# Kernel tuning notes

Measured on AMD Instinct MI355X. Metric: run time of the kernel, lower is better.

The kernel has to match this reference:

```python
import math
import jax, jax.numpy as jnp
import numpy as np

EPS = 1e-6
N = 20000
KS = [256, 128, 64, 32]
DS = [1, 3, 5, 7]  # 2l+1 for l=0..3


def setup_inputs() -> dict:
    key = jax.random.key(0)
    ks = jax.random.split(key, 16)
    inp = {}
    for l, (d, k) in enumerate(zip(DS, KS)):
        inp[f"f{l}"] = jax.random.normal(ks[l], (N, d, d, k), dtype=jnp.float32)
        inp[f"wr{l}"] = jnp.ones((k,), dtype=jnp.float32)
        inp[f"wi{l}"] = jax.random.normal(ks[4 + l], (k, k), dtype=jnp.float32) / math.sqrt(k)
        inp[f"wo{l}"] = jax.random.normal(ks[8 + l], (k, k), dtype=jnp.float32) / math.sqrt(k)
    return inp


def _rmsnorm(x, w):
    # equivariant RMSNorm: RMS over uncoupled (i,j) dims and channels, per atom
    inv = jax.lax.rsqrt(jnp.mean(x * x, axis=(-3, -2, -1), keepdims=True) + EPS)
    return x * inv * w


def _linear(x, w):
    # channel mixing on last axis: [n,i,j,f] x [f,g] -> [n,i,j,g]
    return jnp.einsum('nijf,fg->nijg', x, w)


def _tp(u):
    # tensor product in uncoupled basis, per-channel matmul over (i,j)
    d = max(u.shape[-2], 1)
    return jnp.einsum('nijf,njkf->nikf', u, u) / math.sqrt(d)


def _cg_iter(f, wr, wi, wo):
    h = _linear(_rmsnorm(f, wr), wi)
    return f + _linear(_tp(h), wo)


def reference(f0, f1, f2, f3, wr0, wr1, wr2, wr3, wi0, wi1, wi2, wi3, wo0, wo1, wo2, wo3):
    feats = (f0, f1, f2, f3)
    wrs = (wr0, wr1, wr2, wr3)
    wis = (wi0, wi1, wi2, wi3)
    wos = (wo0, wo1, wo2, wo3)
    return tuple(_cg_iter(f, wr, wi, wo) for f, wr, wi, wo in zip(feats, wrs, wis, wos))
```

## Files before the change

kernel.cpp:

```cpp
#include <hip/hip_runtime.h>
#include <math.h>

#define BLOCK 256

typedef __attribute__((ext_vector_type(8))) short bf16x8;
typedef __attribute__((ext_vector_type(4))) float f32x4;
typedef __attribute__((ext_vector_type(16))) float f32x16;

static __device__ __forceinline__ unsigned short f2bf(float x) {
  unsigned u = __builtin_bit_cast(unsigned, x);
  u = (u + 0x7FFFu + ((u >> 16) & 1u)) >> 16;
  return (unsigned short)u;
}
static __device__ __forceinline__ float bf2f(unsigned short b) {
  return __builtin_bit_cast(float, (unsigned)b << 16);
}

typedef __attribute__((address_space(1))) unsigned int as1_t;
typedef __attribute__((address_space(3))) unsigned int as3_t;
static __device__ __forceinline__ void gl2lds16(const void* g, void* l) {
  __builtin_amdgcn_global_load_lds((const as1_t*)g, (as3_t*)l, 16, 0, 0);
}

__global__ __launch_bounds__(BLOCK) void prep_w(
    const float* __restrict__ w0, const float* __restrict__ w1,
    const float* __restrict__ w2, const float* __restrict__ w3,
    const float* __restrict__ w4, const float* __restrict__ w5,
    const float* __restrict__ w6, const float* __restrict__ w7,
    unsigned short* __restrict__ wsU)
{
  const int bpm[8]  = {64, 64, 16, 16, 4, 4, 1, 1};
  const int ks[8]   = {256, 256, 128, 128, 64, 64, 32, 32};
  const size_t doffE[8] = {0ull, 81920ull, 163840ull, 184320ull,
                           204800ull, 209920ull, 215040ull, 216576ull};
  const int cse[8] = {10240, 10240, 5120, 5120, 2560, 2560, 1536, 1536};
  const float* srcs[8] = {w0, w1, w2, w3, w4, w5, w6, w7};

  int m = 0, sub = blockIdx.x;
  while (m < 7 && sub >= bpm[m]) { sub -= bpm[m]; ++m; }
  const int K = ks[m];
  const int e = sub * 1024 + threadIdx.x * 4;
  const float4 v = *(const float4*)&srcs[m][e];
  const int k = e / K, c = e % K;
  const size_t d0 = doffE[m] + (size_t)(k >> 5) * cse[m] + (size_t)c * 40 + (k & 31);
  wsU[d0]       = f2bf(v.x);
  wsU[d0 + 40]  = f2bf(v.y);
  wsU[d0 + 80]  = f2bf(v.z);
  wsU[d0 + 120] = f2bf(v.w);
}

template<int K, int MP, int MR, int SX, int CG, int MODE, int CH, int PCH>
__device__ __forceinline__ void gemm_run(
    int tid, unsigned short* XB, const char* __restrict__ wsrc,
    const char* __restrict__ nextW, unsigned char* WT,
    const float* __restrict__ fres, float* __restrict__ outg, size_t obase)
{
  constexpr int RG = 4 / CG;
  constexpr int MT = MP / 32, NT = K / 32;
  constexpr int MTW = (MT + RG - 1) / RG, NTW = NT / CG;
  const int lane = tid & 63, wave = tid >> 6;
  const int wgn = wave % CG, wgm = wave / CG;
  const int rA = lane & 31, hA = lane >> 5;

  f32x16 acc[MTW][NTW] = {};

  for (int kc = 0; kc < CH; ++kc) {
    const unsigned short* W16 = (const unsigned short*)WT;
    bf16x8 bfr[NTW][2], afr[MTW][2];
#pragma unroll
    for (int ni = 0; ni < NTW; ++ni)
#pragma unroll
      for (int q = 0; q < 2; ++q)
        bfr[ni][q] = *(const bf16x8*)&W16[((wgn + ni * CG) * 32 + rA) * 40 + q * 16 + hA * 8];
#pragma unroll
    for (int mi = 0; mi < MTW; ++mi) {
      const int mt = wgm + mi * RG;
      if (mt < MT) {
#pragma unroll
        for (int q = 0; q < 2; ++q)
          afr[mi][q] = *(const bf16x8*)&XB[(mt * 32 + rA) * SX + kc * 32 + q * 16 + hA * 8];
      }
    }
    __syncthreads();

    if (kc + 1 < CH) {
      const char* sp = wsrc + (size_t)(kc + 1) * PCH;
      for (int o = wave * 1024; o < PCH; o += 4096)
        gl2lds16(sp + o + lane * 16, WT + o);
    } else if (nextW) {
      for (int o = wave * 1024; o < PCH; o += 4096)
        gl2lds16(nextW + o + lane * 16, WT + o);
    }

#pragma unroll
    for (int mi = 0; mi < MTW; ++mi) {
      const int mt = wgm + mi * RG;
      if (mt < MT) {
#pragma unroll
        for (int ni = 0; ni < NTW; ++ni)
#pragma unroll
          for (int q = 0; q < 2; ++q)
            acc[mi][ni] = __builtin_amdgcn_mfma_f32_32x32x16_bf16(
                afr[mi][q], bfr[ni][q], acc[mi][ni], 0, 0, 0);
      }
    }
    __syncthreads();
  }

#pragma unroll
  for (int mi = 0; mi < MTW; ++mi) {
    const int mt = wgm + mi * RG;
    if (mt >= MT) continue;
#pragma unroll
    for (int ni = 0; ni < NTW; ++ni) {
      const int col = (wgn + ni * CG) * 32 + rA;
#pragma unroll
      for (int r = 0; r < 16; ++r) {
        const int row = mt * 32 + (r & 3) + ((r >> 2) << 3) + (hA << 2);
        const float v = acc[mi][ni][r];
        if constexpr (MODE == 0) {
          if (row < MR) XB[row * SX + col] = f2bf(v);
        } else if constexpr (MODE == 2) {
          if (row < MR) XB[row * SX + col] = f2bf(v * v);
        } else {
          if (row < MR) {
            const size_t o = obase + (size_t)row * K + col;
            outg[o] = fres[o] + v;
          }
        }
      }
    }
  }
}

template<int K, int MP, int MR, int SX, int CG, int MODE, int CSE>
__device__ __forceinline__ void gemm_res(
    int tid, unsigned short* XB, const unsigned short* __restrict__ W16,
    const float* __restrict__ fres, float* __restrict__ outg, size_t obase)
{
  constexpr int RG = 4 / CG;
  constexpr int MT = MP / 32, NT = K / 32;
  constexpr int MTW = (MT + RG - 1) / RG, NTW = NT / CG;
  constexpr int CH = K / 32;
  const int lane = tid & 63, wave = tid >> 6;
  const int wgn = wave % CG, wgm = wave / CG;
  const int rA = lane & 31, hA = lane >> 5;

  f32x16 acc[MTW][NTW] = {};

#pragma unroll
  for (int kc = 0; kc < CH; ++kc) {
    const unsigned short* Wc = W16 + kc * CSE;
    bf16x8 bfr[NTW][2], afr[MTW][2];
#pragma unroll
    for (int ni = 0; ni < NTW; ++ni)
#pragma unroll
      for (int q = 0; q < 2; ++q)
        bfr[ni][q] = *(const bf16x8*)&Wc[((wgn + ni * CG) * 32 + rA) * 40 + q * 16 + hA * 8];
#pragma unroll
    for (int mi = 0; mi < MTW; ++mi) {
      const int mt = wgm + mi * RG;
      if (mt < MT) {
#pragma unroll
        for (int q = 0; q < 2; ++q)
          afr[mi][q] = *(const bf16x8*)&XB[(mt * 32 + rA) * SX + kc * 32 + q * 16 + hA * 8];
      }
    }
#pragma unroll
    for (int mi = 0; mi < MTW; ++mi) {
      const int mt = wgm + mi * RG;
      if (mt < MT) {
#pragma unroll
        for (int ni = 0; ni < NTW; ++ni)
#pragma unroll
          for (int q = 0; q < 2; ++q)
            acc[mi][ni] = __builtin_amdgcn_mfma_f32_32x32x16_bf16(
                afr[mi][q], bfr[ni][q], acc[mi][ni], 0, 0, 0);
      }
    }
  }

  if constexpr (MODE != 3) __syncthreads();

#pragma unroll
  for (int mi = 0; mi < MTW; ++mi) {
    const int mt = wgm + mi * RG;
    if (mt >= MT) continue;
#pragma unroll
    for (int ni = 0; ni < NTW; ++ni) {
      const int col = (wgn + ni * CG) * 32 + rA;
#pragma unroll
      for (int r = 0; r < 16; ++r) {
        const int row = mt * 32 + (r & 3) + ((r >> 2) << 3) + (hA << 2);
        const float v = acc[mi][ni][r];
        if constexpr (MODE == 0) {
          if (row < MR) XB[row * SX + col] = f2bf(v);
        } else if constexpr (MODE == 2) {
          if (row < MR) XB[row * SX + col] = f2bf(v * v);
        } else {
          if (row < MR) {
            const size_t o = obase + (size_t)row * K + col;
            outg[o] = fres[o] + v;
          }
        }
      }
    }
  }
}

template<int D, int K, int A, int MP, int CG, int CH, int PCH, int MODE1>
__device__ __forceinline__ void cg_body(
    int bid, const float* __restrict__ f, const float* __restrict__ wr,
    const char* __restrict__ wiw, const char* __restrict__ wow,
    float* __restrict__ out, unsigned char* SMEM)
{
  constexpr int DD  = D * D;
  constexpr int MR  = A * DD;
  constexpr int SX  = K + 8;
  constexpr int TPA = BLOCK / A;
  constexpr int NF4 = DD * K / 4;
  constexpr int CEIL = (NF4 + TPA - 1) / TPA;
  constexpr int XBB = MP * SX * 2;

  unsigned short* XB = (unsigned short*)SMEM;
  unsigned char*  WT = SMEM + XBB;

  const int tid = threadIdx.x, lane = tid & 63, wave = tid >> 6;
  const int nbase = bid * A;
  const size_t obase = (size_t)nbase * DD * K;

  for (int o = wave * 1024; o < PCH; o += 4096)
    gl2lds16(wiw + o + lane * 16, WT + o);

  const int a = tid / TPA, j = tid % TPA;
  const float* fa = f + (size_t)(nbase + a) * DD * K;
  float4 vreg[CEIL];
  float ss = 0.f;
#pragma unroll
  for (int it = 0; it < CEIL; ++it) {
    const int i = j + it * TPA;
    if (i < NF4) {
      vreg[it] = *(const float4*)&fa[i * 4];
      ss += vreg[it].x * vreg[it].x + vreg[it].y * vreg[it].y +
            vreg[it].z * vreg[it].z + vreg[it].w * vreg[it].w;
    }
  }
#pragma unroll
  for (int o = TPA >> 1; o >= 1; o >>= 1) ss += __shfl_xor(ss, o, 64);
  const float inv = rsqrtf(ss / (float)(DD * K) + 1e-6f);

#pragma unroll
  for (int it = 0; it < CEIL; ++it) {
    const int i = j + it * TPA;
    if (i < NF4) {
      const int e = i * 4, m = e / K, c = e % K;
      const float4 w4 = *(const float4*)&wr[c];
      const unsigned long long pk =
          (unsigned long long)f2bf(vreg[it].x * inv * w4.x) |
          ((unsigned long long)f2bf(vreg[it].y * inv * w4.y) << 16) |
          ((unsigned long long)f2bf(vreg[it].z * inv * w4.z) << 32) |
          ((unsigned long long)f2bf(vreg[it].w * inv * w4.w) << 48);
      *(unsigned long long*)&XB[(a * DD + m) * SX + c] = pk;
    }
  }
  __syncthreads();

  gemm_run<K, MP, MR, SX, CG, MODE1, CH, PCH>(
      tid, XB, wiw, wow, WT, nullptr, nullptr, 0);
  __syncthreads();

  if constexpr (D > 1) {
    const float rsD = rsqrtf((float)D);
    constexpr int PAIRS = A * K;
    if constexpr (PAIRS >= BLOCK) {
      static_assert(PAIRS % BLOCK == 0, "tp coverage");
#pragma unroll
      for (int it = 0; it < PAIRS / BLOCK; ++it) {
        const int p = tid + it * BLOCK;
        const int aa = p / K, c = p % K;
        float hv[DD];
#pragma unroll
        for (int r = 0; r < DD; ++r) hv[r] = bf2f(XB[(aa * DD + r) * SX + c]);
#pragma unroll
        for (int i2 = 0; i2 < D; ++i2)
#pragma unroll
          for (int k2 = 0; k2 < D; ++k2) {
            float s = 0.f;
#pragma unroll
            for (int jj = 0; jj < D; ++jj) s += hv[i2 * D + jj] * hv[jj * D + k2];
            XB[(aa * DD + i2 * D + k2) * SX + c] = f2bf(s * rsD);
          }
      }
    } else {
      static_assert(PAIRS * 2 == BLOCK, "tp two-lane coverage");
      const int p = tid >> 1, half = tid & 1;
      const int aa = p / K, c = p % K;
      float hv[DD];
#pragma unroll
      for (int r = 0; r < DD; ++r) hv[r] = bf2f(XB[(aa * DD + r) * SX + c]);
      const int i0 = half ? (D / 2 + 1) : 0;
      const int i1 = half ? D : (D / 2 + 1);
      for (int i2 = i0; i2 < i1; ++i2)
#pragma unroll
        for (int k2 = 0; k2 < D; ++k2) {
          float s = 0.f;
#pragma unroll
          for (int jj = 0; jj < D; ++jj) s += hv[i2 * D + jj] * hv[jj * D + k2];
          XB[(aa * DD + i2 * D + k2) * SX + c] = f2bf(s * rsD);
        }
    }
    __syncthreads();
  }

  gemm_run<K, MP, MR, SX, CG, 3, CH, PCH>(
      tid, XB, wow, nullptr, WT, f, out, obase);
}

template<int D, int K, int A, int MP, int CG, int CSE, int WIB, int WOB>
__device__ __forceinline__ void cg_body_res(
    int bid, const float* __restrict__ f, const float* __restrict__ wr,
    const char* __restrict__ wiw, const char* __restrict__ wow,
    float* __restrict__ out, unsigned char* SMEM)
{
  constexpr int DD  = D * D;
  constexpr int MR  = A * DD;
  constexpr int SX  = K + 8;
  constexpr int TPA = BLOCK / A;
  constexpr int NF4 = DD * K / 4;
  constexpr int CEIL = (NF4 + TPA - 1) / TPA;
  constexpr int XBB = MP * SX * 2;

  unsigned short* XB = (unsigned short*)SMEM;
  unsigned char*  W  = SMEM + XBB;

  const int tid = threadIdx.x, lane = tid & 63, wave = tid >> 6;
  const int nbase = bid * A;
  const size_t obase = (size_t)nbase * DD * K;

  for (int o = wave * 1024; o < WIB; o += 4096)
    gl2lds16(wiw + o + lane * 16, W + o);
  for (int o = wave * 1024; o < WOB; o += 4096)
    gl2lds16(wow + o + lane * 16, W + WIB + o);

  const int a = tid / TPA, j = tid % TPA;
  const float* fa = f + (size_t)(nbase + a) * DD * K;
  float4 vreg[CEIL];
  float ss = 0.f;
#pragma unroll
  for (int it = 0; it < CEIL; ++it) {
    const int i = j + it * TPA;
    if (i < NF4) {
      vreg[it] = *(const float4*)&fa[i * 4];
      ss += vreg[it].x * vreg[it].x + vreg[it].y * vreg[it].y +
            vreg[it].z * vreg[it].z + vreg[it].w * vreg[it].w;
    }
  }
#pragma unroll
  for (int o = TPA >> 1; o >= 1; o >>= 1) ss += __shfl_xor(ss, o, 64);
  const float inv = rsqrtf(ss / (float)(DD * K) + 1e-6f);

#pragma unroll
  for (int it = 0; it < CEIL; ++it) {
    const int i = j + it * TPA;
    if (i < NF4) {
      const int e = i * 4, m = e / K, c = e % K;
      const float4 w4 = *(const float4*)&wr[c];
      const unsigned long long pk =
          (unsigned long long)f2bf(vreg[it].x * inv * w4.x) |
          ((unsigned long long)f2bf(vreg[it].y * inv * w4.y) << 16) |
          ((unsigned long long)f2bf(vreg[it].z * inv * w4.z) << 32) |
          ((unsigned long long)f2bf(vreg[it].w * inv * w4.w) << 48);
      *(unsigned long long*)&XB[(a * DD + m) * SX + c] = pk;
    }
  }
  __syncthreads();

  gemm_res<K, MP, MR, SX, CG, 0, CSE>(
      tid, XB, (const unsigned short*)W, nullptr, nullptr, 0);
  __syncthreads();

  {
    const float rsD = rsqrtf((float)D);
    constexpr int PAIRS = A * K;
    if constexpr (PAIRS >= BLOCK) {
      static_assert(PAIRS % BLOCK == 0, "tp coverage");
#pragma unroll
      for (int it = 0; it < PAIRS / BLOCK; ++it) {
        const int p = tid + it * BLOCK;
        const int aa = p / K, c = p % K;
        float hv[DD];
#pragma unroll
        for (int r = 0; r < DD; ++r) hv[r] = bf2f(XB[(aa * DD + r) * SX + c]);
#pragma unroll
        for (int i2 = 0; i2 < D; ++i2)
#pragma unroll
          for (int k2 = 0; k2 < D; ++k2) {
            float s = 0.f;
#pragma unroll
            for (int jj = 0; jj < D; ++jj) s += hv[i2 * D + jj] * hv[jj * D + k2];
            XB[(aa * DD + i2 * D + k2) * SX + c] = f2bf(s * rsD);
          }
      }
    } else {
      static_assert(PAIRS * 2 == BLOCK, "tp two-lane coverage");
      const int p = tid >> 1, half = tid & 1;
      const int aa = p / K, c = p % K;
      float hv[DD];
#pragma unroll
      for (int r = 0; r < DD; ++r) hv[r] = bf2f(XB[(aa * DD + r) * SX + c]);
      const int i0 = half ? (D / 2 + 1) : 0;
      const int i1 = half ? D : (D / 2 + 1);
      for (int i2 = i0; i2 < i1; ++i2)
#pragma unroll
        for (int k2 = 0; k2 < D; ++k2) {
          float s = 0.f;
#pragma unroll
          for (int jj = 0; jj < D; ++jj) s += hv[i2 * D + jj] * hv[jj * D + k2];
          XB[(aa * DD + i2 * D + k2) * SX + c] = f2bf(s * rsD);
        }
    }
  }
  __syncthreads();

  gemm_res<K, MP, MR, SX, CG, 3, CSE>(
      tid, XB, (const unsigned short*)(W + WIB), f, out, obase);
}

__global__ __launch_bounds__(BLOCK, 3) void cg_mega(
    const float* __restrict__ f0, const float* __restrict__ wr0,
    const float* __restrict__ f1, const float* __restrict__ wr1,
    const float* __restrict__ f2, const float* __restrict__ wr2,
    const float* __restrict__ f3, const float* __restrict__ wr3,
    const char* __restrict__ wsB,
    float* __restrict__ out0, float* __restrict__ out1,
    float* __restrict__ out2, float* __restrict__ out3)
{
  __shared__ __align__(16) unsigned char SMEM[53760];
  const int b = blockIdx.x;
  if (b < 625) {
    cg_body<1, 256, 32,  32, 4, 8, 20480, 2>(
        b, f0, wr0, wsB + 0, wsB + 163840, out0, SMEM);
  } else if (b < 1875) {
    cg_body<3, 128, 16, 160, 4, 4, 10240, 0>(
        b - 625, f1, wr1, wsB + 327680, wsB + 368640, out1, SMEM);
  } else if (b < 4375) {
    cg_body_res<5,  64, 8, 224, 2, 2560, 10240, 10240>(
        b - 1875, f2, wr2, wsB + 409600, wsB + 419840, out2, SMEM);
  } else {
    cg_body_res<7,  32, 8, 416, 1, 1536,  3072,  3072>(
        b - 4375, f3, wr3, wsB + 430080, wsB + 433152, out3, SMEM);
  }
}

template<int K, int MP, int MR, int SX, int SH, int WGM, int WGN, int MTW, int NTW, bool FINAL>
__device__ __forceinline__ void fb_gemm(
    int tid, const unsigned short* __restrict__ XB, float* __restrict__ Hs,
    unsigned short* __restrict__ WTl, const float* __restrict__ Wg,
    const float* __restrict__ fres, float* __restrict__ out, size_t obase)
{
  constexpr int TM = MP / 16;
  constexpr int WSTR = 40;
  const int lane = tid & 63;
  const int wave = tid >> 6;
  const int wgn = wave % WGN;
  const int wgm = wave / WGN;
  const int rl = lane & 15;
  const int kl = (lane >> 4) * 8;
  const int rit = (lane >> 4) * 4;
  const int cit = lane & 15;

  f32x4 acc[MTW][NTW];
#pragma unroll
  for (int mi = 0; mi < MTW; ++mi)
#pragma unroll
    for (int ni = 0; ni < NTW; ++ni) acc[mi][ni] = f32x4{0.f, 0.f, 0.f, 0.f};

  for (int kc = 0; kc < K / 32; ++kc) {
    __syncthreads();
    for (int i = tid; i < 32 * K; i += BLOCK) {
      const int kk = i / K, c = i % K;
      WTl[c * WSTR + kk] = f2bf(Wg[(size_t)(kc * 32 + kk) * K + c]);
    }
    __syncthreads();
    bf16x8 bfr[NTW], afr[MTW];
#pragma unroll
    for (int ni = 0; ni < NTW; ++ni) {
      const int col = (wgn + ni * WGN) * 16 + rl;
      bfr[ni] = *(const bf16x8*)&WTl[col * WSTR + kl];
    }
#pragma unroll
    for (int mi = 0; mi < MTW; ++mi) {
      const int mt = wgm + mi * WGM;
      if (mt < TM) afr[mi] = *(const bf16x8*)&XB[(mt * 16 + rl) * SX + kc * 32 + kl];
    }
#pragma unroll
    for (int mi = 0; mi < MTW; ++mi) {
      const int mt = wgm + mi * WGM;
      if (mt < TM) {
#pragma unroll
        for (int ni = 0; ni < NTW; ++ni)
          acc[mi][ni] = __builtin_amdgcn_mfma_f32_16x16x32_bf16(afr[mi], bfr[ni], acc[mi][ni], 0, 0, 0);
      }
    }
  }
#pragma unroll
  for (int mi = 0; mi < MTW; ++mi) {
    const int mt = wgm + mi * WGM;
    if (mt >= TM) continue;
#pragma unroll
    for (int ni = 0; ni < NTW; ++ni) {
      const int col = (wgn + ni * WGN) * 16 + cit;
#pragma unroll
      for (int r = 0; r < 4; ++r) {
        const int row = mt * 16 + rit + r;
        if constexpr (!FINAL) {
          Hs[row * SH + col] = acc[mi][ni][r];
        } else {
          if (row < MR) {
            const size_t o = obase + (size_t)row * K + col;
            out[o] = fres[o] + acc[mi][ni][r];
          }
        }
      }
    }
  }
}

template<int D, int K, int A, int MP, int WGM, int WGN, int MTW, int NTW>
__global__ __launch_bounds__(BLOCK) void cg_mfma_fb(
    const float* __restrict__ f, const float* __restrict__ wr,
    const float* __restrict__ wi, const float* __restrict__ wo,
    float* __restrict__ out)
{
  constexpr int DD = D * D;
  constexpr int MR = A * DD;
  constexpr int SX = K + 8;
  constexpr int SH = K + 4;
  constexpr int TPA = BLOCK / A;
  constexpr int WSTR = 40;

  __shared__ __align__(16) unsigned short XB[MP * SX];
  __shared__ __align__(16) float H[MP * SH];
  __shared__ __align__(16) unsigned short WTl[K * WSTR];
  __shared__ float s_inv[A];

  const int tid = threadIdx.x;
  const int nbase = blockIdx.x * A;
  const size_t obase = (size_t)nbase * DD * K;

  if constexpr (MP > MR) {
    for (int i = tid; i < (MP - MR) * K; i += BLOCK)
      XB[(MR + i / K) * SX + (i % K)] = 0;
  }
  {
    const int a = tid / TPA, j = tid % TPA;
    const float4* fap = (const float4*)(f + (size_t)(nbase + a) * DD * K);
    constexpr int NF4 = DD * K / 4;
    float ss = 0.f;
    for (int i = j; i < NF4; i += TPA) {
      const float4 v = fap[i];
      const int e = i * 4, m = e / K, c = e % K;
      *(float4*)&H[(a * DD + m) * SH + c] = v;
      ss += v.x * v.x + v.y * v.y + v.z * v.z + v.w * v.w;
    }
#pragma unroll
    for (int o = TPA >> 1; o >= 1; o >>= 1) ss += __shfl_xor(ss, o, 64);
    if (j == 0) s_inv[a] = rsqrtf(ss / (float)(DD * K) + 1e-6f);
  }
  __syncthreads();
  for (int i2 = tid; i2 < MR * K / 2; i2 += BLOCK) {
    const int e = i2 * 2, m = e / K, c = e % K;
    const float2 v = *(const float2*)&H[m * SH + c];
    const float2 wv = *(const float2*)&wr[c];
    const float s = s_inv[m / DD];
    const unsigned lo = f2bf(v.x * s * wv.x);
    const unsigned hi = f2bf(v.y * s * wv.y);
    *(unsigned*)&XB[m * SX + c] = lo | (hi << 16);
  }
  fb_gemm<K, MP, MR, SX, SH, WGM, WGN, MTW, NTW, false>(
      tid, XB, H, WTl, wi, nullptr, nullptr, 0);
  __syncthreads();
  {
    const float rsD = rsqrtf((float)D);
    for (int base = 0; base < A * K; base += BLOCK) {
      const int t2 = base + tid;
      if (t2 < A * K) {
        const int aa = t2 / K, c = t2 % K;
        float hv[DD];
#pragma unroll
        for (int r = 0; r < DD; ++r) hv[r] = H[(aa * DD + r) * SH + c];
#pragma unroll
        for (int i = 0; i < D; ++i)
#pragma unroll
          for (int k2 = 0; k2 < D; ++k2) {
            float s = 0.f;
#pragma unroll
            for (int jj = 0; jj < D; ++jj) s += hv[i * D + jj] * hv[jj * D + k2];
            XB[(aa * DD + i * D + k2) * SX + c] = f2bf(s * rsD);
          }
      }
    }
  }
  fb_gemm<K, MP, MR, SX, SH, WGM, WGN, MTW, NTW, true>(
      tid, XB, nullptr, WTl, wo, f, out, obase);
}

extern "C" void kernel_launch(void* const* d_in, const int* in_sizes, int n_in,
                              void* d_out, int out_size, void* d_ws, size_t ws_size,
                              hipStream_t stream)
{
  (void)in_sizes; (void)n_in; (void)out_size;
  const float* f0  = (const float*)d_in[0];
  const float* wr0 = (const float*)d_in[1];
  const float* wi0 = (const float*)d_in[2];
  const float* wo0 = (const float*)d_in[3];
  const float* f1  = (const float*)d_in[4];
  const float* wr1 = (const float*)d_in[5];
  const float* wi1 = (const float*)d_in[6];
  const float* wo1 = (const float*)d_in[7];
  const float* f2  = (const float*)d_in[8];
  const float* wr2 = (const float*)d_in[9];
  const float* wi2 = (const float*)d_in[10];
  const float* wo2 = (const float*)d_in[11];
  const float* f3  = (const float*)d_in[12];
  const float* wr3 = (const float*)d_in[13];
  const float* wi3 = (const float*)d_in[14];
  const float* wo3 = (const float*)d_in[15];

  float* out  = (float*)d_out;
  float* out0 = out;
  float* out1 = out0 + (size_t)20000 * 256;
  float* out2 = out1 + (size_t)20000 * 1152;
  float* out3 = out2 + (size_t)20000 * 1600;

  if (ws_size >= 436224) {
    unsigned short* wsU = (unsigned short*)d_ws;
    const char* wsB = (const char*)d_ws;
    prep_w<<<170, BLOCK, 0, stream>>>(wi0, wo0, wi1, wo1, wi2, wo2, wi3, wo3, wsU);
    cg_mega<<<6875, BLOCK, 0, stream>>>(
        f0, wr0, f1, wr1, f2, wr2, f3, wr3, wsB, out0, out1, out2, out3);
  } else {
    cg_mfma_fb<1, 256, 32,  32, 1, 4, 2, 4><<< 625, BLOCK, 0, stream>>>(f0, wr0, wi0, wo0, out0);
    cg_mfma_fb<3, 128,  8,  80, 1, 4, 5, 2><<<2500, BLOCK, 0, stream>>>(f1, wr1, wi1, wo1, out1);
    cg_mfma_fb<5,  64,  4, 112, 1, 4, 7, 1><<<5000, BLOCK, 0, stream>>>(f2, wr2, wi2, wo2, out2);
    cg_mfma_fb<7,  32,  4, 208, 4, 1, 4, 2><<<5000, BLOCK, 0, stream>>>(f3, wr3, wi3, wo3, out3);
  }
}
```

Measured before the change: 254.0 us.

## Stage weight slices per wave and drop block barriers in streamed GEMM loop

Each wave now stages into LDS only the weight column slices it reads itself, so the per-chunk __syncthreads are replaced with wave-local s_waitcnt vmcnt/lgkmcnt waits. This aims to remove block-wide barrier stalls in the K-chunk loop and let waves progress independently, overlapping the next chunk's global-to-LDS load with the MFMAs. The cost is a tighter correctness dependency: it relies on each wave owning disjoint slices and on the waitcnt ordering. It also skips the trailing barrier for the residual-output mode.

```diff
diff --git a/kernel.cpp b/kernel.cpp
--- a/kernel.cpp
+++ b/kernel.cpp
@@ -20,6 +20,34 @@
 typedef __attribute__((address_space(3))) unsigned int as3_t;
 static __device__ __forceinline__ void gl2lds16(const void* g, void* l) {
   __builtin_amdgcn_global_load_lds((const as1_t*)g, (as3_t*)l, 16, 0, 0);
+}
+static __device__ __forceinline__ void gl2lds4(const void* g, void* l) {
+  __builtin_amdgcn_global_load_lds((const as1_t*)g, (as3_t*)l, 4, 0, 0);
+}
+
+template<int BYTES>
+static __device__ __forceinline__ void stage_wave(
+    const char* src, unsigned char* dst, int lane) {
+  constexpr int N16 = BYTES / 1024;
+  constexpr int REM = BYTES - N16 * 1024;
+#pragma unroll
+  for (int j = 0; j < N16; ++j)
+    gl2lds16(src + j * 1024 + lane * 16, dst + j * 1024);
+#pragma unroll
+  for (int j = 0; j < REM / 256; ++j)
+    gl2lds4(src + N16 * 1024 + j * 256 + lane * 4, dst + N16 * 1024 + j * 256);
+}
+
+template<int K, int CG>
+static __device__ __forceinline__ void stage_slices(
+    const char* src, unsigned char* WT, int wave, int lane) {
+  constexpr int NTW = (K / 32) / CG;
+  const int wgn = wave % CG;
+#pragma unroll
+  for (int ni = 0; ni < NTW; ++ni) {
+    const int off = (wgn + ni * CG) * 2560;
+    stage_wave<2560>(src + off, WT + off, lane);
+  }
 }
 
 __global__ __launch_bounds__(BLOCK) void prep_w(
@@ -50,7 +78,7 @@
 }
 
 template<int K, int MP, int MR, int SX, int CG, int MODE, int CH, int PCH>
-__device__ __forceinline__ void gemm_run(
+__device__ __forceinline__ void gemm_stream(
     int tid, unsigned short* XB, const char* __restrict__ wsrc,
     const char* __restrict__ nextW, unsigned char* WT,
     const float* __restrict__ fres, float* __restrict__ outg, size_t obase)
@@ -65,6 +93,7 @@
   f32x16 acc[MTW][NTW] = {};
 
   for (int kc = 0; kc < CH; ++kc) {
+    asm volatile("s_waitcnt vmcnt(0)" ::: "memory");
     const unsigned short* W16 = (const unsigned short*)WT;
     bf16x8 bfr[NTW][2], afr[MTW][2];
 #pragma unroll
@@ -81,17 +110,13 @@
           afr[mi][q] = *(const bf16x8*)&XB[(mt * 32 + rA) * SX + kc * 32 + q * 16 + hA * 8];
       }
     }
-    __syncthreads();
-
+    asm volatile("s_waitcnt lgkmcnt(0)" ::: "memory");
+    __builtin_amdgcn_sched_barrier(0);
     if (kc + 1 < CH) {
-      const char* sp = wsrc + (size_t)(kc + 1) * PCH;
-      for (int o = wave * 1024; o < PCH; o += 4096)
-        gl2lds16(sp + o + lane * 16, WT + o);
+      stage_slices<K, CG>(wsrc + (size_t)(kc + 1) * PCH, WT, wave, lane);
     } else if (nextW) {
-      for (int o = wave * 1024; o < PCH; o += 4096)
-        gl2lds16(nextW + o + lane * 16, WT + o);
-    }
-
+      stage_slices<K, CG>(nextW, WT, wave, lane);
+    }
 #pragma unroll
     for (int mi = 0; mi < MTW; ++mi) {
       const int mt = wgm + mi * RG;
@@ -104,8 +129,9 @@
                 afr[mi][q], bfr[ni][q], acc[mi][ni], 0, 0, 0);
       }
     }
-    __syncthreads();
-  }
+  }
+
+  if constexpr (MODE != 3) __syncthreads();
 
 #pragma unroll
   for (int mi = 0; mi < MTW; ++mi) {
@@ -229,8 +255,7 @@
   const int nbase = bid * A;
   const size_t obase = (size_t)nbase * DD * K;
 
-  for (int o = wave * 1024; o < PCH; o += 4096)
-    gl2lds16(wiw + o + lane * 16, WT + o);
+  stage_slices<K, CG>(wiw, WT, wave, lane);
 
   const int a = tid / TPA, j = tid % TPA;
   const float* fa = f + (size_t)(nbase + a) * DD * K;
@@ -265,7 +290,7 @@
   }
   __syncthreads();
 
-  gemm_run<K, MP, MR, SX, CG, MODE1, CH, PCH>(
+  gemm_stream<K, MP, MR, SX, CG, MODE1, CH, PCH>(
       tid, XB, wiw, wow, WT, nullptr, nullptr, 0);
   __syncthreads();
 
@@ -312,7 +337,7 @@
     __syncthreads();
   }
 
-  gemm_run<K, MP, MR, SX, CG, 3, CH, PCH>(
+  gemm_stream<K, MP, MR, SX, CG, 3, CH, PCH>(
       tid, XB, wow, nullptr, WT, f, out, obase);
 }
 
```

New measurement: 252.3 us. No clear change (-0.6%).
